# Performance work log

Hardware: AMD Instinct MI355X
Metric: run time of the kernel (lower is better)

The kernel has to match this reference:

```python
import jax, jax.numpy as jnp
import numpy as np

B, S, D, N, H = 4, 1024, 768, 12, 64
IGNORE = -100000.0


def setup_inputs() -> dict:
    key = jax.random.key(0)
    ks = jax.random.split(key, 9)
    std = 0.02
    return {
        "normalized_resid_pre": jax.random.normal(ks[0], (B, S, D), dtype=jnp.float32),
        "W_Q": jax.random.normal(ks[1], (N, D, H), dtype=jnp.float32) * std,
        "W_K": jax.random.normal(ks[2], (N, D, H), dtype=jnp.float32) * std,
        "W_V": jax.random.normal(ks[3], (N, D, H), dtype=jnp.float32) * std,
        "W_O": jax.random.normal(ks[4], (N, H, D), dtype=jnp.float32) * std,
        "b_Q": jnp.zeros((N, H), dtype=jnp.float32),
        "b_K": jnp.zeros((N, H), dtype=jnp.float32),
        "b_V": jnp.zeros((N, H), dtype=jnp.float32),
        "b_O": jnp.zeros((D,), dtype=jnp.float32),
    }


def reference(normalized_resid_pre, W_Q, W_K, W_V, W_O, b_Q, b_K, b_V, b_O):
    x = normalized_resid_pre  # [b, s, d]
    d_head = W_Q.shape[-1]
    # per-head projections: [b, n, s, h]
    Q = jnp.einsum("bsd,ndh->bnsh", x, W_Q) + b_Q[None, :, None, :]
    K = jnp.einsum("bsd,ndh->bnsh", x, W_K) + b_K[None, :, None, :]
    V = jnp.einsum("bsd,ndh->bnsh", x, W_V) + b_V[None, :, None, :]
    # scores [b, n, s_q, s_k]
    scores = jnp.einsum("bnqh,bnkh->bnqk", Q, K) / jnp.sqrt(jnp.float32(d_head))
    s = scores.shape[-1]
    # original: tril(scores) + triu(IGNORE, k=1) == where(causal, scores, IGNORE)
    causal = jnp.tril(jnp.ones((s, s), dtype=bool))
    masked = jnp.where(causal[None, None], scores, jnp.float32(IGNORE))
    probs = jax.nn.softmax(masked, axis=-1)
    # z [b, s_q, n, h]
    z = jnp.einsum("bnqk,bnkh->bqnh", probs, V)
    out = jnp.einsum("bqnh,nhd->bqd", z, W_O) + b_O
    return out
```

## Files before the change

### kernel.cpp

```cpp
#include <hip/hip_runtime.h>

typedef __bf16 bf16x8 __attribute__((ext_vector_type(8)));
typedef __bf16 bf16x4 __attribute__((ext_vector_type(4)));
typedef float  f32x4  __attribute__((ext_vector_type(4)));

constexpr int B_ = 4, S_ = 1024, D_ = 768, N_ = 12, H_ = 64;
constexpr int BNSH = B_ * N_ * S_ * H_;
constexpr float SCALE2 = 0.18033688011f;

__device__ __forceinline__ f32x4 mfma16(bf16x8 a, bf16x8 b, f32x4 c) {
    return __builtin_amdgcn_mfma_f32_16x16x32_bf16(a, b, c, 0, 0, 0);
}

__device__ __forceinline__ void gload16(const __bf16* g, __bf16* l) {
    __builtin_amdgcn_global_load_lds(
        (const __attribute__((address_space(1))) unsigned int*)g,
        (__attribute__((address_space(3))) unsigned int*)l, 16, 0, 0);
}

__device__ __forceinline__ void stage128x64(const __bf16* g, int ld, __bf16* lds,
                                            int wid, int lane) {
    #pragma unroll
    for (int i = 0; i < 4; ++i) {
        int cb = (wid * 4 + i) * 64;
        int chunk = cb + lane;
        int r = chunk >> 3, p = chunk & 7;
        int q = p ^ (r & 7);
        gload16(g + (size_t)r * ld + q * 8, lds + cb * 8);
    }
}
__device__ __forceinline__ void stage64x64(const __bf16* g, int ld, __bf16* lds,
                                           int wid, int lane) {
    #pragma unroll
    for (int i = 0; i < 2; ++i) {
        int cb = (wid * 2 + i) * 64;
        int chunk = cb + lane;
        int r = chunk >> 3, p = chunk & 7;
        int q = p ^ (r & 7);
        gload16(g + (size_t)r * ld + q * 8, lds + cb * 8);
    }
}

template <int CTRL>
__device__ __forceinline__ float dpp_mov(float x) {
    return __int_as_float(__builtin_amdgcn_update_dpp(
        0, __float_as_int(x), CTRL, 0xf, 0xf, true));
}
__device__ __forceinline__ float red16_max(float x) {
    x = fmaxf(x, dpp_mov<0xB1>(x));
    x = fmaxf(x, dpp_mov<0x4E>(x));
    x = fmaxf(x, dpp_mov<0x124>(x));
    x = fmaxf(x, dpp_mov<0x128>(x));
    return x;
}
__device__ __forceinline__ float red16_sum(float x) {
    x += dpp_mov<0xB1>(x);
    x += dpp_mov<0x4E>(x);
    x += dpp_mov<0x124>(x);
    x += dpp_mov<0x128>(x);
    return x;
}

__global__ __launch_bounds__(256) void prep_kernel(
    const float* __restrict__ x,
    const float* __restrict__ wq, const float* __restrict__ wk,
    const float* __restrict__ wv, const float* __restrict__ wo,
    __bf16* __restrict__ xb, __bf16* __restrict__ wt, __bf16* __restrict__ wot) {
    __shared__ __bf16 T[64][65];
    const int blk = blockIdx.x;
    const int tid = threadIdx.x;
    if (blk < 768) {
        int base = blk * 1024 + tid;
        #pragma unroll
        for (int i = 0; i < 4; ++i) {
            int idx = base + i * 256;
            float4 v = ((const float4*)x)[idx];
            bf16x4 o;
            o[0] = (__bf16)v.x; o[1] = (__bf16)v.y;
            o[2] = (__bf16)v.z; o[3] = (__bf16)v.w;
            ((bf16x4*)xb)[idx] = o;
        }
        return;
    }
    int rr = tid >> 4, c4 = (tid & 15) * 4;
    if (blk < 1200) {
        int t = blk - 768;
        int dt = t % 12, mh = t / 12;
        int mat = mh / 12, n = mh % 12;
        const float* in = (mat == 0 ? wq : mat == 1 ? wk : wv) + (size_t)n * 768 * 64;
        __bf16* outp = wt + (size_t)(mat * 768 + n * 64) * 768;
        int d0 = dt * 64;
        #pragma unroll
        for (int i = 0; i < 4; ++i) {
            int row = rr + 16 * i;
            float4 v = *(const float4*)&in[(size_t)(d0 + row) * 64 + c4];
            T[c4 + 0][row] = (__bf16)v.x;
            T[c4 + 1][row] = (__bf16)v.y;
            T[c4 + 2][row] = (__bf16)v.z;
            T[c4 + 3][row] = (__bf16)v.w;
        }
        __syncthreads();
        #pragma unroll
        for (int i = 0; i < 4; ++i) {
            int hrow = rr + 16 * i;
            bf16x4 o;
            o[0] = T[hrow][c4 + 0]; o[1] = T[hrow][c4 + 1];
            o[2] = T[hrow][c4 + 2]; o[3] = T[hrow][c4 + 3];
            *(bf16x4*)&outp[(size_t)hrow * 768 + d0 + c4] = o;
        }
    } else {
        int t = blk - 1200;
        int r0 = (t % 12) * 64, c0 = (t / 12) * 64;
        #pragma unroll
        for (int i = 0; i < 4; ++i) {
            int row = rr + 16 * i;
            float4 v = *(const float4*)&wo[(size_t)(r0 + row) * 768 + c0 + c4];
            T[c4 + 0][row] = (__bf16)v.x;
            T[c4 + 1][row] = (__bf16)v.y;
            T[c4 + 2][row] = (__bf16)v.z;
            T[c4 + 3][row] = (__bf16)v.w;
        }
        __syncthreads();
        #pragma unroll
        for (int i = 0; i < 4; ++i) {
            int crow = rr + 16 * i;
            bf16x4 o;
            o[0] = T[crow][c4 + 0]; o[1] = T[crow][c4 + 1];
            o[2] = T[crow][c4 + 2]; o[3] = T[crow][c4 + 3];
            *(bf16x4*)&wot[(size_t)(c0 + crow) * 768 + r0 + c4] = o;
        }
    }
}

__global__ __launch_bounds__(256) void qkv_gemm(
    const __bf16* __restrict__ xb, const __bf16* __restrict__ wtg,
    const float* __restrict__ bq, const float* __restrict__ bk,
    const float* __restrict__ bv,
    __bf16* __restrict__ Qb, __bf16* __restrict__ Kb, __bf16* __restrict__ Vtb) {
    __shared__ __bf16 As[2][128 * 64];
    __shared__ __bf16 Bs[2][64 * 64];
    const int m0 = blockIdx.x * 128;
    const int j0 = blockIdx.y * 64;
    const int tid = threadIdx.x, wid = tid >> 6, lane = tid & 63;
    const int quad = lane >> 4, lrow = lane & 15;
    const int l3 = lrow & 7;
    int koff[2];
    #pragma unroll
    for (int ks = 0; ks < 2; ++ks)
        koff[ks] = lrow * 64 + ((ks * 4 + quad) ^ l3) * 8;

    f32x4 zf = {0.f, 0.f, 0.f, 0.f};
    f32x4 acc[2][4];
    #pragma unroll
    for (int i = 0; i < 2; ++i)
        #pragma unroll
        for (int j = 0; j < 4; ++j) acc[i][j] = zf;

    stage128x64(xb + (size_t)m0 * 768, 768, As[0], wid, lane);
    stage64x64(wtg + (size_t)j0 * 768, 768, Bs[0], wid, lane);

    for (int kt = 0; kt < 12; ++kt) {
        const int buf = kt & 1;
        __syncthreads();
        if (kt < 11) {
            stage128x64(xb + (size_t)m0 * 768 + (kt + 1) * 64, 768, As[buf ^ 1], wid, lane);
            stage64x64(wtg + (size_t)j0 * 768 + (kt + 1) * 64, 768, Bs[buf ^ 1], wid, lane);
        }
        #pragma unroll
        for (int ks = 0; ks < 2; ++ks) {
            bf16x8 af[2], bfr[4];
            #pragma unroll
            for (int mi = 0; mi < 2; ++mi)
                af[mi] = *(const bf16x8*)(As[buf] + (wid * 32 + mi * 16) * 64 + koff[ks]);
            #pragma unroll
            for (int ni = 0; ni < 4; ++ni)
                bfr[ni] = *(const bf16x8*)(Bs[buf] + ni * 1024 + koff[ks]);
            #pragma unroll
            for (int mi = 0; mi < 2; ++mi)
                #pragma unroll
                for (int ni = 0; ni < 4; ++ni)
                    acc[mi][ni] = mfma16(af[mi], bfr[ni], acc[mi][ni]);
        }
    }

    const int mat = j0 / 768;
    const int n = (j0 % 768) >> 6;
    const int b = m0 >> 10;
    const int s_base = (m0 & 1023) + wid * 32;
    const float* bias = (mat == 0 ? bq : mat == 1 ? bk : bv) + n * 64;
    float bias_v[4];
    #pragma unroll
    for (int ni = 0; ni < 4; ++ni) bias_v[ni] = bias[ni * 16 + lrow];

    if (mat == 2) {
        __bf16* vout = Vtb + (size_t)(b * N_ + n) * 64 * 1024;
        #pragma unroll
        for (int mi = 0; mi < 2; ++mi)
            #pragma unroll
            for (int ni = 0; ni < 4; ++ni) {
                int h = ni * 16 + lrow;
                int s0 = s_base + mi * 16 + quad * 4;
                bf16x4 pv;
                #pragma unroll
                for (int r = 0; r < 4; ++r)
                    pv[r] = (__bf16)(acc[mi][ni][r] + bias_v[ni]);
                *(bf16x4*)(vout + (size_t)h * 1024 + s0) = pv;
            }
    } else {
        __bf16* qk = (mat == 0 ? Qb : Kb) + (size_t)(b * N_ + n) * 1024 * 64;
        #pragma unroll
        for (int mi = 0; mi < 2; ++mi)
            #pragma unroll
            for (int r = 0; r < 4; ++r) {
                int s = s_base + mi * 16 + quad * 4 + r;
                #pragma unroll
                for (int ni = 0; ni < 4; ++ni)
                    qk[(size_t)s * 64 + ni * 16 + lrow] =
                        (__bf16)(acc[mi][ni][r] + bias_v[ni]);
            }
    }
}

__global__ __launch_bounds__(256) void attn_mfma(
    const __bf16* __restrict__ Qb, const __bf16* __restrict__ Kb,
    const __bf16* __restrict__ Vtb, __bf16* __restrict__ zb) {
    __shared__ __bf16 Ks[2][64 * 64], Vs[2][64 * 64];
    __shared__ __bf16 Ps[4][16 * 64];
    const int bid = blockIdx.x;
    const int qt = 15 - bid / 48;
    const int bn = bid % 48;
    const int b = bn / N_, n = bn % N_;
    const int tid = threadIdx.x, wid = tid >> 6, lane = tid & 63;
    const int quad = lane >> 4, lrow = lane & 15;
    const int l3 = lrow & 7;
    const __bf16* Qg = Qb + (size_t)(b * N_ + n) * S_ * H_;
    const __bf16* Kg = Kb + (size_t)(b * N_ + n) * S_ * H_;
    const __bf16* Vg = Vtb + (size_t)(b * N_ + n) * H_ * S_;
    const int q0 = qt * 64;

    int koff[2];
    #pragma unroll
    for (int ks = 0; ks < 2; ++ks)
        koff[ks] = lrow * 64 + ((ks * 4 + quad) ^ l3) * 8;
    int pw[4][4];
    #pragma unroll
    for (int nt = 0; nt < 4; ++nt)
        #pragma unroll
        for (int r = 0; r < 4; ++r) {
            int row = quad * 4 + r, col = nt * 16 + lrow;
            pw[nt][r] = row * 64 + ((col >> 3) ^ (row & 7)) * 8 + (col & 7);
        }

    bf16x8 qf[2];
    #pragma unroll
    for (int ks = 0; ks < 2; ++ks)
        qf[ks] = *(const bf16x8*)&Qg[(size_t)(q0 + wid * 16 + lrow) * 64
                                     + (ks * 4 + quad) * 8];

    stage64x64(Kg, 64, Ks[0], wid, lane);
    stage64x64(Vg, 1024, Vs[0], wid, lane);

    f32x4 zf = {0.f, 0.f, 0.f, 0.f};
    f32x4 o[4];
    float m_r[4], l_r[4];
    #pragma unroll
    for (int i = 0; i < 4; ++i) { o[i] = zf; m_r[i] = -1e30f; l_r[i] = 0.f; }
    __bf16* Pw = Ps[wid];

    auto do_tile = [&](int buf, bool diag) {
        f32x4 sc[4];
        #pragma unroll
        for (int nt = 0; nt < 4; ++nt) sc[nt] = zf;
        #pragma unroll
        for (int ks = 0; ks < 2; ++ks) {
            #pragma unroll
            for (int nt = 0; nt < 4; ++nt) {
                bf16x8 kf = *(const bf16x8*)(Ks[buf] + nt * 1024 + koff[ks]);
                sc[nt] = mfma16(qf[ks], kf, sc[nt]);
            }
        }
        float v[4][4];
        #pragma unroll
        for (int nt = 0; nt < 4; ++nt)
            #pragma unroll
            for (int r = 0; r < 4; ++r) v[nt][r] = sc[nt][r] * SCALE2;
        if (diag) {
            #pragma unroll
            for (int nt = 0; nt < 4; ++nt)
                #pragma unroll
                for (int r = 0; r < 4; ++r)
                    if ((nt * 16 + lrow) > (wid * 16 + quad * 4 + r))
                        v[nt][r] = -1e30f;
        }
        float alpha[4];
        #pragma unroll
        for (int r = 0; r < 4; ++r) {
            float mt = fmaxf(fmaxf(v[0][r], v[1][r]), fmaxf(v[2][r], v[3][r]));
            mt = red16_max(mt);
            float mn = fmaxf(m_r[r], mt);
            alpha[r] = exp2f(m_r[r] - mn);
            m_r[r] = mn;
            float rs = 0.f;
            #pragma unroll
            for (int nt = 0; nt < 4; ++nt) {
                float p = exp2f(v[nt][r] - mn);
                v[nt][r] = p;
                rs += p;
            }
            rs = red16_sum(rs);
            l_r[r] = l_r[r] * alpha[r] + rs;
        }
        #pragma unroll
        for (int ht = 0; ht < 4; ++ht)
            #pragma unroll
            for (int r = 0; r < 4; ++r) o[ht][r] *= alpha[r];
        #pragma unroll
        for (int nt = 0; nt < 4; ++nt)
            #pragma unroll
            for (int r = 0; r < 4; ++r) Pw[pw[nt][r]] = (__bf16)v[nt][r];
        #pragma unroll
        for (int ks = 0; ks < 2; ++ks) {
            bf16x8 ap = *(const bf16x8*)(Pw + koff[ks]);
            #pragma unroll
            for (int ht = 0; ht < 4; ++ht) {
                bf16x8 vf = *(const bf16x8*)(Vs[buf] + ht * 1024 + koff[ks]);
                o[ht] = mfma16(ap, vf, o[ht]);
            }
        }
    };

    for (int kt = 0; kt < qt; ++kt) {
        __syncthreads();
        stage64x64(Kg + (size_t)(kt + 1) * 64 * 64, 64, Ks[(kt + 1) & 1], wid, lane);
        stage64x64(Vg + (kt + 1) * 64, 1024, Vs[(kt + 1) & 1], wid, lane);
        do_tile(kt & 1, false);
    }
    __syncthreads();
    do_tile(qt & 1, true);

    __bf16* zout = zb + (size_t)b * S_ * 768 + (size_t)n * 64;
    #pragma unroll
    for (int r = 0; r < 4; ++r) {
        float linv = 1.0f / l_r[r];
        int q = q0 + wid * 16 + quad * 4 + r;
        #pragma unroll
        for (int ht = 0; ht < 4; ++ht)
            zout[(size_t)q * 768 + ht * 16 + lrow] = (__bf16)(o[ht][r] * linv);
    }
}

__global__ __launch_bounds__(256) void out_gemm(
    const __bf16* __restrict__ zb, const __bf16* __restrict__ wot,
    const float* __restrict__ bo, float* __restrict__ out) {
    __shared__ __bf16 As[2][128 * 64];
    __shared__ __bf16 Bs[2][64 * 64];
    const int m0 = blockIdx.x * 128;
    const int j0 = blockIdx.y * 64;
    const int tid = threadIdx.x, wid = tid >> 6, lane = tid & 63;
    const int quad = lane >> 4, lrow = lane & 15;
    const int l3 = lrow & 7;
    int koff[2];
    #pragma unroll
    for (int ks = 0; ks < 2; ++ks)
        koff[ks] = lrow * 64 + ((ks * 4 + quad) ^ l3) * 8;

    f32x4 zf = {0.f, 0.f, 0.f, 0.f};
    f32x4 acc[2][4];
    #pragma unroll
    for (int i = 0; i < 2; ++i)
        #pragma unroll
        for (int j = 0; j < 4; ++j) acc[i][j] = zf;

    stage128x64(zb + (size_t)m0 * 768, 768, As[0], wid, lane);
    stage64x64(wot + (size_t)j0 * 768, 768, Bs[0], wid, lane);

    for (int kt = 0; kt < 12; ++kt) {
        const int buf = kt & 1;
        __syncthreads();
        if (kt < 11) {
            stage128x64(zb + (size_t)m0 * 768 + (kt + 1) * 64, 768, As[buf ^ 1], wid, lane);
            stage64x64(wot + (size_t)j0 * 768 + (kt + 1) * 64, 768, Bs[buf ^ 1], wid, lane);
        }
        #pragma unroll
        for (int ks = 0; ks < 2; ++ks) {
            bf16x8 af[2], bfr[4];
            #pragma unroll
            for (int mi = 0; mi < 2; ++mi)
                af[mi] = *(const bf16x8*)(As[buf] + (wid * 32 + mi * 16) * 64 + koff[ks]);
            #pragma unroll
            for (int ni = 0; ni < 4; ++ni)
                bfr[ni] = *(const bf16x8*)(Bs[buf] + ni * 1024 + koff[ks]);
            #pragma unroll
            for (int mi = 0; mi < 2; ++mi)
                #pragma unroll
                for (int ni = 0; ni < 4; ++ni)
                    acc[mi][ni] = mfma16(af[mi], bfr[ni], acc[mi][ni]);
        }
    }

    float bias_v[4];
    #pragma unroll
    for (int ni = 0; ni < 4; ++ni) bias_v[ni] = bo[j0 + ni * 16 + lrow];
    #pragma unroll
    for (int mi = 0; mi < 2; ++mi)
        #pragma unroll
        for (int r = 0; r < 4; ++r) {
            int m = m0 + wid * 32 + mi * 16 + quad * 4 + r;
            #pragma unroll
            for (int ni = 0; ni < 4; ++ni)
                out[(size_t)m * 768 + j0 + ni * 16 + lrow] =
                    acc[mi][ni][r] + bias_v[ni];
        }
}

extern "C" void kernel_launch(void* const* d_in, const int* in_sizes, int n_in,
                              void* d_out, int out_size, void* d_ws, size_t ws_size,
                              hipStream_t stream) {
    const float* x  = (const float*)d_in[0];
    const float* wq = (const float*)d_in[1];
    const float* wk = (const float*)d_in[2];
    const float* wv = (const float*)d_in[3];
    const float* wo = (const float*)d_in[4];
    const float* bq = (const float*)d_in[5];
    const float* bk = (const float*)d_in[6];
    const float* bv = (const float*)d_in[7];
    const float* bo = (const float*)d_in[8];
    float* out = (float*)d_out;

    __bf16* p   = (__bf16*)d_ws;
    __bf16* xb  = p;  p += (size_t)4096 * 768;
    __bf16* wt  = p;  p += (size_t)2304 * 768;
    __bf16* wot = p;  p += (size_t)768 * 768;
    __bf16* Qb  = p;  p += (size_t)BNSH;
    __bf16* Kb  = p;  p += (size_t)BNSH;
    __bf16* Vtb = p;  p += (size_t)BNSH;
    __bf16* zb  = p;  p += (size_t)4096 * 768;

    prep_kernel<<<1344, 256, 0, stream>>>(x, wq, wk, wv, wo, xb, wt, wot);
    qkv_gemm<<<dim3(32, 36), 256, 0, stream>>>(xb, wt, bq, bk, bv, Qb, Kb, Vtb);
    attn_mfma<<<768, 256, 0, stream>>>(Qb, Kb, Vtb, zb);
    out_gemm<<<dim3(32, 12), 256, 0, stream>>>(zb, wot, bo, out);
}
```

Before: 147.1 us.

## Enlarge QKV GEMM tile and transpose attention MFMA to per-lane rows

The QKV GEMM now computes a 128x128 output tile per block, with a 2x2 warp layout and a 4x4 accumulator grid per warp, which halves the grid and improves operand reuse. The attention kernel swaps MFMA operand order so each lane owns one query row. Softmax row max and sum then reduce in-lane plus two cross-lane shuffles instead of per-row DPP reductions, and the P tile and z output are written as packed bf16x4 vectors. The softmax scale is folded into Q once at load rather than applied to every score tile. This uses more registers and LDS in the GEMM, which may lower occupancy, and the fewer GEMM blocks may underfill the CUs.

After: 156.6 us. 1.06x slower.

```diff
diff --git a/kernel.cpp b/kernel.cpp
--- a/kernel.cpp
+++ b/kernel.cpp
@@ -39,26 +39,6 @@
         int q = p ^ (r & 7);
         gload16(g + (size_t)r * ld + q * 8, lds + cb * 8);
     }
-}
-
-template <int CTRL>
-__device__ __forceinline__ float dpp_mov(float x) {
-    return __int_as_float(__builtin_amdgcn_update_dpp(
-        0, __float_as_int(x), CTRL, 0xf, 0xf, true));
-}
-__device__ __forceinline__ float red16_max(float x) {
-    x = fmaxf(x, dpp_mov<0xB1>(x));
-    x = fmaxf(x, dpp_mov<0x4E>(x));
-    x = fmaxf(x, dpp_mov<0x124>(x));
-    x = fmaxf(x, dpp_mov<0x128>(x));
-    return x;
-}
-__device__ __forceinline__ float red16_sum(float x) {
-    x += dpp_mov<0xB1>(x);
-    x += dpp_mov<0x4E>(x);
-    x += dpp_mov<0x124>(x);
-    x += dpp_mov<0x128>(x);
-    return x;
 }
 
 __global__ __launch_bounds__(256) void prep_kernel(
@@ -138,55 +118,57 @@
     const float* __restrict__ bv,
     __bf16* __restrict__ Qb, __bf16* __restrict__ Kb, __bf16* __restrict__ Vtb) {
     __shared__ __bf16 As[2][128 * 64];
-    __shared__ __bf16 Bs[2][64 * 64];
+    __shared__ __bf16 Bs[2][128 * 64];
     const int m0 = blockIdx.x * 128;
-    const int j0 = blockIdx.y * 64;
+    const int j0 = blockIdx.y * 128;
     const int tid = threadIdx.x, wid = tid >> 6, lane = tid & 63;
     const int quad = lane >> 4, lrow = lane & 15;
     const int l3 = lrow & 7;
+    const int wr = wid & 1, wc = wid >> 1;
     int koff[2];
     #pragma unroll
     for (int ks = 0; ks < 2; ++ks)
         koff[ks] = lrow * 64 + ((ks * 4 + quad) ^ l3) * 8;
 
     f32x4 zf = {0.f, 0.f, 0.f, 0.f};
-    f32x4 acc[2][4];
-    #pragma unroll
-    for (int i = 0; i < 2; ++i)
+    f32x4 acc[4][4];
+    #pragma unroll
+    for (int i = 0; i < 4; ++i)
         #pragma unroll
         for (int j = 0; j < 4; ++j) acc[i][j] = zf;
 
     stage128x64(xb + (size_t)m0 * 768, 768, As[0], wid, lane);
-    stage64x64(wtg + (size_t)j0 * 768, 768, Bs[0], wid, lane);
+    stage128x64(wtg + (size_t)j0 * 768, 768, Bs[0], wid, lane);
 
     for (int kt = 0; kt < 12; ++kt) {
         const int buf = kt & 1;
         __syncthreads();
         if (kt < 11) {
             stage128x64(xb + (size_t)m0 * 768 + (kt + 1) * 64, 768, As[buf ^ 1], wid, lane);
-            stage64x64(wtg + (size_t)j0 * 768 + (kt + 1) * 64, 768, Bs[buf ^ 1], wid, lane);
+            stage128x64(wtg + (size_t)j0 * 768 + (kt + 1) * 64, 768, Bs[buf ^ 1], wid, lane);
         }
         #pragma unroll
         for (int ks = 0; ks < 2; ++ks) {
-            bf16x8 af[2], bfr[4];
-            #pragma unroll
-            for (int mi = 0; mi < 2; ++mi)
-                af[mi] = *(const bf16x8*)(As[buf] + (wid * 32 + mi * 16) * 64 + koff[ks]);
+            bf16x8 af[4], bfr[4];
+            #pragma unroll
+            for (int mi = 0; mi < 4; ++mi)
+                af[mi] = *(const bf16x8*)(As[buf] + (wr * 64 + mi * 16) * 64 + koff[ks]);
             #pragma unroll
             for (int ni = 0; ni < 4; ++ni)
-                bfr[ni] = *(const bf16x8*)(Bs[buf] + ni * 1024 + koff[ks]);
-            #pragma unroll
-            for (int mi = 0; mi < 2; ++mi)
+                bfr[ni] = *(const bf16x8*)(Bs[buf] + (wc * 64 + ni * 16) * 64 + koff[ks]);
+            #pragma unroll
+            for (int mi = 0; mi < 4; ++mi)
                 #pragma unroll
                 for (int ni = 0; ni < 4; ++ni)
                     acc[mi][ni] = mfma16(af[mi], bfr[ni], acc[mi][ni]);
         }
     }
 
-    const int mat = j0 / 768;
-    const int n = (j0 % 768) >> 6;
+    const int jw = j0 + wc * 64;
+    const int mat = jw / 768;
+    const int n = (jw % 768) >> 6;
     const int b = m0 >> 10;
-    const int s_base = (m0 & 1023) + wid * 32;
+    const int s_base = (m0 & 1023) + wr * 64;
     const float* bias = (mat == 0 ? bq : mat == 1 ? bk : bv) + n * 64;
     float bias_v[4];
     #pragma unroll
@@ -195,7 +177,7 @@
     if (mat == 2) {
         __bf16* vout = Vtb + (size_t)(b * N_ + n) * 64 * 1024;
         #pragma unroll
-        for (int mi = 0; mi < 2; ++mi)
+        for (int mi = 0; mi < 4; ++mi)
             #pragma unroll
             for (int ni = 0; ni < 4; ++ni) {
                 int h = ni * 16 + lrow;
@@ -209,7 +191,7 @@
     } else {
         __bf16* qk = (mat == 0 ? Qb : Kb) + (size_t)(b * N_ + n) * 1024 * 64;
         #pragma unroll
-        for (int mi = 0; mi < 2; ++mi)
+        for (int mi = 0; mi < 4; ++mi)
             #pragma unroll
             for (int r = 0; r < 4; ++r) {
                 int s = s_base + mi * 16 + quad * 4 + r;
@@ -225,7 +207,7 @@
     const __bf16* __restrict__ Qb, const __bf16* __restrict__ Kb,
     const __bf16* __restrict__ Vtb, __bf16* __restrict__ zb) {
     __shared__ __bf16 Ks[2][64 * 64], Vs[2][64 * 64];
-    __shared__ __bf16 Ps[4][16 * 64];
+    __shared__ __bf16 Pt[4][16 * 64];
     const int bid = blockIdx.x;
     const int qt = 15 - bid / 48;
     const int bn = bid % 48;
@@ -242,30 +224,37 @@
     #pragma unroll
     for (int ks = 0; ks < 2; ++ks)
         koff[ks] = lrow * 64 + ((ks * 4 + quad) ^ l3) * 8;
-    int pw[4][4];
-    #pragma unroll
-    for (int nt = 0; nt < 4; ++nt)
-        #pragma unroll
-        for (int r = 0; r < 4; ++r) {
-            int row = quad * 4 + r, col = nt * 16 + lrow;
-            pw[nt][r] = row * 64 + ((col >> 3) ^ (row & 7)) * 8 + (col & 7);
-        }
+    int ptw[4], ptr_[2];
+    #pragma unroll
+    for (int nt = 0; nt < 4; ++nt) {
+        int c16 = nt * 2 + (quad >> 1);
+        ptw[nt] = lrow * 64 + (c16 ^ l3) * 8 + (quad & 1) * 4;
+    }
+    #pragma unroll
+    for (int ks = 0; ks < 2; ++ks)
+        ptr_[ks] = lrow * 64 + ((ks * 4 + quad) ^ l3) * 8;
 
     bf16x8 qf[2];
     #pragma unroll
-    for (int ks = 0; ks < 2; ++ks)
-        qf[ks] = *(const bf16x8*)&Qg[(size_t)(q0 + wid * 16 + lrow) * 64
-                                     + (ks * 4 + quad) * 8];
+    for (int ks = 0; ks < 2; ++ks) {
+        bf16x8 raw = *(const bf16x8*)&Qg[(size_t)(q0 + wid * 16 + lrow) * 64
+                                         + ks * 32 + quad * 8];
+        bf16x8 sc8;
+        #pragma unroll
+        for (int j = 0; j < 8; ++j) sc8[j] = (__bf16)((float)raw[j] * SCALE2);
+        qf[ks] = sc8;
+    }
 
     stage64x64(Kg, 64, Ks[0], wid, lane);
     stage64x64(Vg, 1024, Vs[0], wid, lane);
 
     f32x4 zf = {0.f, 0.f, 0.f, 0.f};
     f32x4 o[4];
-    float m_r[4], l_r[4];
-    #pragma unroll
-    for (int i = 0; i < 4; ++i) { o[i] = zf; m_r[i] = -1e30f; l_r[i] = 0.f; }
-    __bf16* Pw = Ps[wid];
+    #pragma unroll
+    for (int i = 0; i < 4; ++i) o[i] = zf;
+    float m_r = -1e30f, l_r = 0.f;
+    __bf16* Pw = Pt[wid];
+    const int myq = wid * 16 + lrow;
 
     auto do_tile = [&](int buf, bool diag) {
         f32x4 sc[4];
@@ -275,56 +264,57 @@
         for (int ks = 0; ks < 2; ++ks) {
             #pragma unroll
             for (int nt = 0; nt < 4; ++nt) {
-                bf16x8 kf = *(const bf16x8*)(Ks[buf] + nt * 1024 + koff[ks]);
-                sc[nt] = mfma16(qf[ks], kf, sc[nt]);
+                bf16x8 kfr = *(const bf16x8*)(Ks[buf] + nt * 1024 + koff[ks]);
+                sc[nt] = mfma16(kfr, qf[ks], sc[nt]);
             }
         }
-        float v[4][4];
-        #pragma unroll
-        for (int nt = 0; nt < 4; ++nt)
-            #pragma unroll
-            for (int r = 0; r < 4; ++r) v[nt][r] = sc[nt][r] * SCALE2;
         if (diag) {
             #pragma unroll
             for (int nt = 0; nt < 4; ++nt)
                 #pragma unroll
                 for (int r = 0; r < 4; ++r)
-                    if ((nt * 16 + lrow) > (wid * 16 + quad * 4 + r))
-                        v[nt][r] = -1e30f;
-        }
-        float alpha[4];
-        #pragma unroll
-        for (int r = 0; r < 4; ++r) {
-            float mt = fmaxf(fmaxf(v[0][r], v[1][r]), fmaxf(v[2][r], v[3][r]));
-            mt = red16_max(mt);
-            float mn = fmaxf(m_r[r], mt);
-            alpha[r] = exp2f(m_r[r] - mn);
-            m_r[r] = mn;
-            float rs = 0.f;
-            #pragma unroll
-            for (int nt = 0; nt < 4; ++nt) {
-                float p = exp2f(v[nt][r] - mn);
-                v[nt][r] = p;
+                    if ((nt * 16 + quad * 4 + r) > myq) sc[nt][r] = -1e30f;
+        }
+        float mt = -1e30f;
+        #pragma unroll
+        for (int nt = 0; nt < 4; ++nt)
+            #pragma unroll
+            for (int r = 0; r < 4; ++r) mt = fmaxf(mt, sc[nt][r]);
+        mt = fmaxf(mt, __shfl_xor(mt, 16));
+        mt = fmaxf(mt, __shfl_xor(mt, 32));
+        float mn = fmaxf(m_r, mt);
+        float alpha = __builtin_amdgcn_exp2f(m_r - mn);
+        m_r = mn;
+        float rs = 0.f;
+        #pragma unroll
+        for (int nt = 0; nt < 4; ++nt)
+            #pragma unroll
+            for (int r = 0; r < 4; ++r) {
+                float p = __builtin_amdgcn_exp2f(sc[nt][r] - mn);
+                sc[nt][r] = p;
                 rs += p;
             }
-            rs = red16_sum(rs);
-            l_r[r] = l_r[r] * alpha[r] + rs;
-        }
+        rs += __shfl_xor(rs, 16);
+        rs += __shfl_xor(rs, 32);
+        l_r = l_r * alpha + rs;
         #pragma unroll
         for (int ht = 0; ht < 4; ++ht)
             #pragma unroll
-            for (int r = 0; r < 4; ++r) o[ht][r] *= alpha[r];
-        #pragma unroll
-        for (int nt = 0; nt < 4; ++nt)
-            #pragma unroll
-            for (int r = 0; r < 4; ++r) Pw[pw[nt][r]] = (__bf16)v[nt][r];
+            for (int r = 0; r < 4; ++r) o[ht][r] *= alpha;
+        #pragma unroll
+        for (int nt = 0; nt < 4; ++nt) {
+            bf16x4 pk;
+            #pragma unroll
+            for (int r = 0; r < 4; ++r) pk[r] = (__bf16)sc[nt][r];
+            *(bf16x4*)(Pw + ptw[nt]) = pk;
+        }
         #pragma unroll
         for (int ks = 0; ks < 2; ++ks) {
-            bf16x8 ap = *(const bf16x8*)(Pw + koff[ks]);
+            bf16x8 pf = *(const bf16x8*)(Pw + ptr_[ks]);
             #pragma unroll
             for (int ht = 0; ht < 4; ++ht) {
-                bf16x8 vf = *(const bf16x8*)(Vs[buf] + ht * 1024 + koff[ks]);
-                o[ht] = mfma16(ap, vf, o[ht]);
+                bf16x8 vfr = *(const bf16x8*)(Vs[buf] + ht * 1024 + koff[ks]);
+                o[ht] = mfma16(vfr, pf, o[ht]);
             }
         }
     };
@@ -338,14 +328,14 @@
     __syncthreads();
     do_tile(qt & 1, true);
 
-    __bf16* zout = zb + (size_t)b * S_ * 768 + (size_t)n * 64;
-    #pragma unroll
-    for (int r = 0; r < 4; ++r) {
-        float linv = 1.0f / l_r[r];
-        int q = q0 + wid * 16 + quad * 4 + r;
-        #pragma unroll
-        for (int ht = 0; ht < 4; ++ht)
-            zout[(size_t)q * 768 + ht * 16 + lrow] = (__bf16)(o[ht][r] * linv);
+    const float linv = 1.0f / l_r;
+    __bf16* zout = zb + (size_t)b * S_ * 768 + (size_t)(q0 + myq) * 768 + n * 64;
+    #pragma unroll
+    for (int ht = 0; ht < 4; ++ht) {
+        bf16x4 zo;
+        #pragma unroll
+        for (int r = 0; r < 4; ++r) zo[r] = (__bf16)(o[ht][r] * linv);
+        *(bf16x4*)&zout[ht * 16 + quad * 4] = zo;
     }
 }
 
@@ -437,7 +427,7 @@
     __bf16* zb  = p;  p += (size_t)4096 * 768;
 
     prep_kernel<<<1344, 256, 0, stream>>>(x, wq, wk, wv, wo, xb, wt, wot);
-    qkv_gemm<<<dim3(32, 36), 256, 0, stream>>>(xb, wt, bq, bk, bv, Qb, Kb, Vtb);
+    qkv_gemm<<<dim3(32, 18), 256, 0, stream>>>(xb, wt, bq, bk, bv, Qb, Kb, Vtb);
     attn_mfma<<<768, 256, 0, stream>>>(Qb, Kb, Vtb, zb);
     out_gemm<<<dim3(32, 12), 256, 0, stream>>>(zb, wot, bo, out);
 }
```
